# Kernel tuning notes

Measured on AMD Instinct MI355X. Metric: run time of the kernel, lower is better.

## Reference

```python
import jax, jax.numpy as jnp
import numpy as np

D1, D2, ADD1, ADD2 = 32, 32, 16, 16
BATCH = 8


def _photon_basis(m, p):
    """All occupation tuples of m modes with p photons, first mode counts descending."""
    basis = []
    def gen(modes, rem, prefix):
        if modes == 1:
            basis.append(prefix + (rem,))
            return
        for k in range(rem, -1, -1):
            gen(modes - 1, rem - k, prefix + (k,))
    gen(m, p, ())
    return basis


def _fock_index_map(d1, d2, add1, add2):
    m = d1 + d2 + add1 + add2
    basis = _photon_basis(m, 2)
    index = {s: i for i, s in enumerate(basis)}
    idx = np.empty(d1 * d2, dtype=np.int64)
    for i in range(d1):
        for j in range(d2):
            s = [0] * m
            s[add1 + i] = 1
            s[add1 + d1 + j] = 1
            idx[i * d2 + j] = index[tuple(s)]
    return idx, len(basis)  # len(basis) == m*(m+1)//2


def setup_inputs() -> dict:
    key = jax.random.key(0)
    idx, fock_dim = _fock_index_map(D1, D2, ADD1, ADD2)
    n = D1 * D2  # 1024
    input_state = jax.random.normal(key, (BATCH, n, n), dtype=jnp.float32)
    return {
        "input_state": input_state,
        "fock_idx": jnp.asarray(idx),   # [n] int64, one Fock index per image-basis element
        "fock_dim": fock_dim,           # static int: 4656
    }


def reference(input_state, fock_idx, fock_dim):
    # P @ rho @ P^T where P[:, c] is one-hot at fock_idx[c].
    # Equivalent to scattering rho[b, i, j] into out[b, fock_idx[i], fock_idx[j]].
    B = input_state.shape[0]
    out = jnp.zeros((B, fock_dim, fock_dim), dtype=input_state.dtype)
    return out.at[:, fock_idx[:, None], fock_idx[None, :]].set(input_state)
```

## Files before the change

### kernel.cpp

```cpp
#include <hip/hip_runtime.h>

constexpr int FOCK_DIM = 4656;
constexpr int N        = 1024;
constexpr int ROW_VEC  = FOCK_DIM / 4;

__global__ void init_inv_kernel(int* __restrict__ inv) {
    int i = blockIdx.x * blockDim.x + threadIdx.x;
    if (i < FOCK_DIM) inv[i] = -1;
}

__global__ void fill_inv_kernel(const int* __restrict__ fock_idx, int* __restrict__ inv) {
    int i = blockIdx.x * blockDim.x + threadIdx.x;
    if (i < N) inv[fock_idx[i]] = i;
}

__global__ __launch_bounds__(256) void scatter_rows_kernel(
    const float* __restrict__ in,
    const int*   __restrict__ inv,
    float*       __restrict__ out) {

    const int br = blockIdx.x;
    const int b  = br / FOCK_DIM;
    const int r  = br - b * FOCK_DIM;
    const int invr = inv[r];

    float4* __restrict__ orow = reinterpret_cast<float4*>(out + (size_t)br * FOCK_DIM);

    if (invr < 0) {
        const float4 z = make_float4(0.f, 0.f, 0.f, 0.f);
        for (int c4 = threadIdx.x; c4 < ROW_VEC; c4 += 256) {
            orow[c4] = z;
        }
        return;
    }

    __shared__ float row[N];
    const float* __restrict__ irow = in + ((size_t)b * N + (size_t)invr) * N;
    for (int i = threadIdx.x; i < N; i += 256) row[i] = irow[i];
    __syncthreads();

    const int4* __restrict__ inv4 = reinterpret_cast<const int4*>(inv);
    for (int c4 = threadIdx.x; c4 < ROW_VEC; c4 += 256) {
        const int4 iv = inv4[c4];
        float4 v;
        v.x = (iv.x >= 0) ? row[iv.x] : 0.f;
        v.y = (iv.y >= 0) ? row[iv.y] : 0.f;
        v.z = (iv.z >= 0) ? row[iv.z] : 0.f;
        v.w = (iv.w >= 0) ? row[iv.w] : 0.f;
        orow[c4] = v;
    }
}

extern "C" void kernel_launch(void* const* d_in, const int* in_sizes, int n_in,
                              void* d_out, int out_size, void* d_ws, size_t ws_size,
                              hipStream_t stream) {
    const float* in       = (const float*)d_in[0];
    const int*   fock_idx = (const int*)d_in[1];
    float*       out      = (float*)d_out;
    int*         inv      = (int*)d_ws;

    const int B = in_sizes[0] / (N * N);

    init_inv_kernel<<<(FOCK_DIM + 255) / 256, 256, 0, stream>>>(inv);
    fill_inv_kernel<<<(N + 255) / 256, 256, 0, stream>>>(fock_idx, inv);
    scatter_rows_kernel<<<B * FOCK_DIM, 256, 0, stream>>>(in, inv, out);
}
```

Measured before the change: 147.3 us.

## Process all batches per row block, merge inverse-map kernels, use nontemporal stores

Each block now handles one Fock row for all batches, staging the input rows in chunks of four batches in shared memory and reusing the inverse-index loads across the batch. The two inverse-map kernels become a single kernel that scans fock_idx once per Fock index, which removes one launch. Output writes use nontemporal stores to avoid polluting the cache with the large output. Batch size is now hard-coded and the grid shrinks to FOCK_DIM blocks, which lowers parallelism and may imbalance work between zero rows and data rows.

```diff
diff --git a/kernel.cpp b/kernel.cpp
--- a/kernel.cpp
+++ b/kernel.cpp
@@ -3,15 +3,21 @@
 constexpr int FOCK_DIM = 4656;
 constexpr int N        = 1024;
 constexpr int ROW_VEC  = FOCK_DIM / 4;
+constexpr int B        = 8;
+constexpr int BCHUNK   = 4;
 
-__global__ void init_inv_kernel(int* __restrict__ inv) {
-    int i = blockIdx.x * blockDim.x + threadIdx.x;
-    if (i < FOCK_DIM) inv[i] = -1;
-}
+typedef float f32x4 __attribute__((ext_vector_type(4)));
+typedef int   i32x4 __attribute__((ext_vector_type(4)));
 
-__global__ void fill_inv_kernel(const int* __restrict__ fock_idx, int* __restrict__ inv) {
-    int i = blockIdx.x * blockDim.x + threadIdx.x;
-    if (i < N) inv[fock_idx[i]] = i;
+__global__ __launch_bounds__(256) void build_inv_kernel(
+    const int* __restrict__ fock_idx, int* __restrict__ inv) {
+    const int f = blockIdx.x * 256 + threadIdx.x;
+    if (f >= FOCK_DIM) return;
+    int r = -1;
+    for (int i = 0; i < N; ++i) {
+        if (fock_idx[i] == f) r = i;
+    }
+    inv[f] = r;
 }
 
 __global__ __launch_bounds__(256) void scatter_rows_kernel(
@@ -19,35 +25,52 @@
     const int*   __restrict__ inv,
     float*       __restrict__ out) {
 
-    const int br = blockIdx.x;
-    const int b  = br / FOCK_DIM;
-    const int r  = br - b * FOCK_DIM;
+    const int r    = blockIdx.x;
+    const int tid  = threadIdx.x;
     const int invr = inv[r];
 
-    float4* __restrict__ orow = reinterpret_cast<float4*>(out + (size_t)br * FOCK_DIM);
-
     if (invr < 0) {
-        const float4 z = make_float4(0.f, 0.f, 0.f, 0.f);
-        for (int c4 = threadIdx.x; c4 < ROW_VEC; c4 += 256) {
-            orow[c4] = z;
+        const f32x4 z = {0.f, 0.f, 0.f, 0.f};
+        const int total4 = B * ROW_VEC;
+        for (int t = tid; t < total4; t += 256) {
+            const int b  = t / ROW_VEC;
+            const int c4 = t - b * ROW_VEC;
+            f32x4* orow = reinterpret_cast<f32x4*>(out + ((size_t)b * FOCK_DIM + r) * FOCK_DIM);
+            __builtin_nontemporal_store(z, orow + c4);
         }
         return;
     }
 
-    __shared__ float row[N];
-    const float* __restrict__ irow = in + ((size_t)b * N + (size_t)invr) * N;
-    for (int i = threadIdx.x; i < N; i += 256) row[i] = irow[i];
-    __syncthreads();
+    __shared__ float rows[BCHUNK][N];
+    const f32x4* __restrict__ in4  = reinterpret_cast<const f32x4*>(in);
+    const i32x4* __restrict__ inv4 = reinterpret_cast<const i32x4*>(inv);
 
-    const int4* __restrict__ inv4 = reinterpret_cast<const int4*>(inv);
-    for (int c4 = threadIdx.x; c4 < ROW_VEC; c4 += 256) {
-        const int4 iv = inv4[c4];
-        float4 v;
-        v.x = (iv.x >= 0) ? row[iv.x] : 0.f;
-        v.y = (iv.y >= 0) ? row[iv.y] : 0.f;
-        v.z = (iv.z >= 0) ? row[iv.z] : 0.f;
-        v.w = (iv.w >= 0) ? row[iv.w] : 0.f;
-        orow[c4] = v;
+    for (int chunk = 0; chunk < B / BCHUNK; ++chunk) {
+        const int b0 = chunk * BCHUNK;
+
+        for (int t = tid; t < BCHUNK * (N / 4); t += 256) {
+            const int bb = t >> 8;
+            const int c  = t & 255;
+            f32x4 v = in4[((size_t)(b0 + bb) * N + (size_t)invr) * (N / 4) + c];
+            reinterpret_cast<f32x4*>(rows[bb])[c] = v;
+        }
+        __syncthreads();
+
+        for (int c4 = tid; c4 < ROW_VEC; c4 += 256) {
+            const i32x4 iv = inv4[c4];
+            #pragma unroll
+            for (int bb = 0; bb < BCHUNK; ++bb) {
+                f32x4 v;
+                v.x = (iv.x >= 0) ? rows[bb][iv.x] : 0.f;
+                v.y = (iv.y >= 0) ? rows[bb][iv.y] : 0.f;
+                v.z = (iv.z >= 0) ? rows[bb][iv.z] : 0.f;
+                v.w = (iv.w >= 0) ? rows[bb][iv.w] : 0.f;
+                f32x4* orow = reinterpret_cast<f32x4*>(
+                    out + ((size_t)(b0 + bb) * FOCK_DIM + r) * FOCK_DIM);
+                __builtin_nontemporal_store(v, orow + c4);
+            }
+        }
+        if (chunk == 0) __syncthreads();
     }
 }
 
@@ -59,9 +82,6 @@
     float*       out      = (float*)d_out;
     int*         inv      = (int*)d_ws;
 
-    const int B = in_sizes[0] / (N * N);
-
-    init_inv_kernel<<<(FOCK_DIM + 255) / 256, 256, 0, stream>>>(inv);
-    fill_inv_kernel<<<(N + 255) / 256, 256, 0, stream>>>(fock_idx, inv);
-    scatter_rows_kernel<<<B * FOCK_DIM, 256, 0, stream>>>(in, inv, out);
+    build_inv_kernel<<<(FOCK_DIM + 255) / 256, 256, 0, stream>>>(fock_idx, inv);
+    scatter_rows_kernel<<<FOCK_DIM, 256, 0, stream>>>(in, inv, out);
 }
```

After: 172.2 us. 1.17x slower.
